# Kernel tuning notes

Hardware: AMD Instinct MI355X
Metric: run time of the kernel (lower is better)

## Reference

```python
import jax, jax.numpy as jnp
import numpy as np

N_ROW = 50000
N_COL = 50000
E = 600000
D = 128
NEG_SLOPE = 0.01  # torch LeakyReLU default


def _leaky(x):
    return jnp.where(x >= 0, x, NEG_SLOPE * x)


def _mlp(x, W1, b1, W2, b2):
    # (Linear -> LeakyReLU) x2, matching nn.Sequential in Conv_layer
    h = _leaky(x @ W1 + b1)
    return _leaky(h @ W2 + b2)


def setup_inputs() -> dict:
    key = jax.random.key(0)
    ks = jax.random.split(key, 16)
    inp = {
        "feat_row": jax.random.normal(ks[0], (N_ROW, D), jnp.float32),
        "feat_col": jax.random.normal(ks[1], (N_COL, D), jnp.float32),
        "src_c2r": jax.random.randint(ks[2], (E,), 0, N_COL, jnp.int32),
        "dst_c2r": jax.random.randint(ks[3], (E,), 0, N_ROW, jnp.int32),
        "w_c2r": jax.random.uniform(ks[4], (E,), jnp.float32),
        "src_r2c": jax.random.randint(ks[5], (E,), 0, N_ROW, jnp.int32),
        "dst_r2c": jax.random.randint(ks[6], (E,), 0, N_COL, jnp.int32),
        "w_r2c": jax.random.uniform(ks[7], (E,), jnp.float32),
        "W1_c2r": jax.random.normal(ks[8], (D, D), jnp.float32) / np.sqrt(D),
        "b1_c2r": jax.random.normal(ks[9], (D,), jnp.float32) * 0.01,
        "W2_c2r": jax.random.normal(ks[10], (D, D), jnp.float32) / np.sqrt(D),
        "b2_c2r": jax.random.normal(ks[11], (D,), jnp.float32) * 0.01,
        "W1_r2c": jax.random.normal(ks[12], (D, D), jnp.float32) / np.sqrt(D),
        "b1_r2c": jax.random.normal(ks[13], (D,), jnp.float32) * 0.01,
        "W2_r2c": jax.random.normal(ks[14], (D, D), jnp.float32) / np.sqrt(D),
        "b2_r2c": jax.random.normal(ks[15], (D,), jnp.float32) * 0.01,
        "eps_c2r": jnp.zeros((), jnp.float32),  # DGL GINConv init_eps=0
        "eps_r2c": jnp.zeros((), jnp.float32),
    }
    return inp


def reference(feat_row, feat_col, src_c2r, dst_c2r, w_c2r, src_r2c, dst_r2c, w_r2c,
              W1_c2r, b1_c2r, W2_c2r, b2_c2r, W1_r2c, b1_r2c, W2_r2c, b2_r2c,
              eps_c2r, eps_r2c):
    # col -> row GINConv (edge-weighted sum aggregation)
    msg = feat_col[src_c2r] * w_c2r[:, None]                       # [E, D]
    agg_row = jax.ops.segment_sum(msg, dst_c2r, num_segments=N_ROW)
    h_row = _mlp((1.0 + eps_c2r) * feat_row + agg_row, W1_c2r, b1_c2r, W2_c2r, b2_c2r)
    # row -> col GINConv using updated row features
    msg2 = h_row[src_r2c] * w_r2c[:, None]                         # [E, D]
    agg_col = jax.ops.segment_sum(msg2, dst_r2c, num_segments=N_COL)
    h_col = _mlp((1.0 + eps_r2c) * feat_col + agg_col, W1_r2c, b1_r2c, W2_r2c, b2_r2c)
    # residual (use_residual=True): add pre-conv embeddings
    return h_row + feat_row, h_col + feat_col
```

## Files before the change

### kernel.cpp

```cpp
#include <hip/hip_runtime.h>
#include <hip/hip_bf16.h>

#define NROW 50000
#define NCOL 50000
#define DDIM 128
#define CAP  32

typedef __bf16 bf16_t;
typedef __bf16 bf16x2 __attribute__((ext_vector_type(2)));
typedef __bf16 bf16x8 __attribute__((ext_vector_type(8)));
typedef float  f32x4  __attribute__((ext_vector_type(4)));

__device__ __forceinline__ float lrelu(float v) { return v >= 0.f ? v : 0.01f * v; }

__device__ __forceinline__ float ldf(const void* p, size_t i, bool f) {
    return f ? ((const float*)p)[i] : (float)((const bf16_t*)p)[i];
}

__device__ __forceinline__ bool dtf(const int* flags, int fi) {
    return (fi == -1) ? true : (fi == -2) ? false : (flags[fi] != 0);
}

struct TensorTab { const void* p[18]; int n[18]; };

__global__ __launch_bounds__(256) void detect_dtypes(TensorTab T, int* flags)
{
    __shared__ int vb, vf;
    const int tid = threadIdx.x;
    const int t = blockIdx.x;
    if (tid == 0) { vb = 0; vf = 0; }
    __syncthreads();
    const int n = T.n[t];
    const bool isFloatArr = (t != 2 && t != 3 && t != 5 && t != 6) && n >= 2;
    if (isFloatArr) {
        int nw = n / 2;
        int wi = (int)(((long long)tid * nw) >> 8);
        unsigned w = ((const unsigned*)T.p[t])[wi];
        unsigned low = w & 0xffffu;
        if (low) {
            int e = (int)((low >> 7) & 0xffu);
            if (e >= 90 && e <= 141) atomicAdd(&vb, 1);
            else                     atomicAdd(&vf, 1);
        }
    }
    __syncthreads();
    if (tid == 0) flags[t] = (isFloatArr && vf > vb) ? 1 : 0;
}

struct WPtrs { const void* W[4]; int fi[4]; };

__global__ __launch_bounds__(256) void prep_all(
    WPtrs P, const int* __restrict__ flags, __bf16* __restrict__ wfp,
    const void* __restrict__ feat, __bf16* __restrict__ cbuf, int n8, int fiFeat,
    int* __restrict__ zc, int zn, int cblocks, int zblocks)
{
    const int b = blockIdx.x;
    const int tid = threadIdx.x;
    if (b < cblocks) {
        int i = b * 256 + tid;
        if (i >= n8) return;
        const bool f = dtf(flags, fiFeat);
        bf16x8 v;
        if (f) {
            f32x4 a = ((const f32x4*)feat)[i * 2];
            f32x4 c = ((const f32x4*)feat)[i * 2 + 1];
#pragma unroll
            for (int j = 0; j < 4; ++j) { v[j] = (__bf16)a[j]; v[j + 4] = (__bf16)c[j]; }
        } else {
            v = ((const bf16x8*)feat)[i];
        }
        ((bf16x8*)cbuf)[i] = v;
    } else if (b < cblocks + zblocks) {
        int i = (b - cblocks) * 256 + tid;
        if (i < zn) zc[i] = 0;
    } else {
        int slot = (b - cblocks - zblocks) * 256 + tid;
        if (slot >= 4 * 2048) return;
        int m = slot >> 11, sIdx = slot & 2047;
        bool f = flags[P.fi[m]] != 0;
        int l = sIdx & 63, combo = sIdx >> 6;
        int ct = combo >> 2, kk = combo & 3;
        int col  = ct * 16 + (l & 15);
        int krow = kk * 32 + (l >> 4) * 8;
        bf16x8 v;
#pragma unroll
        for (int j = 0; j < 8; ++j)
            v[j] = (__bf16)ldf(P.W[m], (size_t)(krow + j) * DDIM + col, f);
        ((bf16x8*)wfp)[slot] = v;
    }
}

__global__ __launch_bounds__(256) void fill_slots_packed(
    const int* __restrict__ dst, const int* __restrict__ srcArr,
    const void* __restrict__ wArr, int nE, int* __restrict__ counts,
    int2* __restrict__ slots2, int* __restrict__ ovCount,
    int* __restrict__ ovList, float* __restrict__ agg,
    const int* __restrict__ flags, int fiW)
{
    int e = blockIdx.x * 256 + threadIdx.x;
    if (e >= nE) return;
    const bool fW = dtf(flags, fiW);
    int d = dst[e];
    int pos = atomicAdd(&counts[d], 1);
    if (pos < CAP) {
        int2 pk;
        pk.x = srcArr[e];
        pk.y = __float_as_int(ldf(wArr, e, fW));
        slots2[(size_t)d * CAP + pos] = pk;
    } else {
        if (pos == CAP) {
            f32x4 z = {0.f, 0.f, 0.f, 0.f};
            f32x4* rp = (f32x4*)(agg + (size_t)d * DDIM);
#pragma unroll 4
            for (int c = 0; c < DDIM / 4; ++c) rp[c] = z;
        }
        int k = atomicAdd(ovCount, 1);
        ovList[k] = e;
    }
}

__global__ __launch_bounds__(256) void segsum_ov(
    const __bf16* __restrict__ gsrc, const int* __restrict__ counts,
    const int2* __restrict__ slots2, float* __restrict__ agg, int nRows,
    const int* __restrict__ srcArr, const int* __restrict__ dstArr,
    const void* __restrict__ wArr, const int* __restrict__ ovList,
    const int* __restrict__ ovCount, const int* __restrict__ flags, int fiW,
    int gblocks)
{
    const int tid  = threadIdx.x;
    const int lane = tid & 63;

    if ((int)blockIdx.x >= gblocks) {
        const bool fW = dtf(flags, fiW);
        const int nOv = *ovCount;
        const int wv_ = tid >> 6;
        const int nWaves = 64 * 4;
        for (int k = (blockIdx.x - gblocks) * 4 + wv_; k < nOv; k += nWaves) {
            int e = ovList[k];
            int s = srcArr[e], d = dstArr[e];
            float wf = ldf(wArr, e, fW);
            bf16x2 v = ((const bf16x2*)gsrc)[(size_t)s * 64 + lane];
            float* ap = agg + (size_t)d * DDIM + lane * 2;
            unsafeAtomicAdd(ap + 0, (float)v[0] * wf);
            unsafeAtomicAdd(ap + 1, (float)v[1] * wf);
        }
        return;
    }

    int row = blockIdx.x * 4 + (tid >> 6);
    if (row >= nRows) return;

    int cntRaw = counts[row];
    int cnt = cntRaw > CAP ? CAP : cntRaw;

    int sr = 0; float wv = 0.f;
    if (lane < cnt) {
        int2 pk = slots2[(size_t)row * CAP + lane];
        sr = pk.x;
        wv = __int_as_float(pk.y);
    }

    float2* ap = (float2*)(agg + (size_t)row * DDIM) + lane;
    float2 acc0 = {0.f, 0.f}, acc1 = {0.f, 0.f};

    const bf16x2* fb = (const bf16x2*)gsrc;
    int i = 0;
    for (; i + 4 <= cnt; i += 4) {
        int   a0 = __shfl(sr, i),     a1 = __shfl(sr, i + 1);
        int   a2 = __shfl(sr, i + 2), a3 = __shfl(sr, i + 3);
        float w0 = __shfl(wv, i),     w1 = __shfl(wv, i + 1);
        float w2 = __shfl(wv, i + 2), w3 = __shfl(wv, i + 3);
        bf16x2 v0 = fb[(size_t)a0 * 64 + lane];
        bf16x2 v1 = fb[(size_t)a1 * 64 + lane];
        bf16x2 v2 = fb[(size_t)a2 * 64 + lane];
        bf16x2 v3 = fb[(size_t)a3 * 64 + lane];
        acc0.x += (float)v0[0] * w0; acc0.y += (float)v0[1] * w0;
        acc1.x += (float)v1[0] * w1; acc1.y += (float)v1[1] * w1;
        acc0.x += (float)v2[0] * w2; acc0.y += (float)v2[1] * w2;
        acc1.x += (float)v3[0] * w3; acc1.y += (float)v3[1] * w3;
    }
    for (; i < cnt; ++i) {
        int   a0 = __shfl(sr, i);
        float w0 = __shfl(wv, i);
        bf16x2 v0 = fb[(size_t)a0 * 64 + lane];
        acc0.x += (float)v0[0] * w0; acc0.y += (float)v0[1] * w0;
    }
    acc0.x += acc1.x; acc0.y += acc1.y;
    if (cntRaw > CAP) {
        unsafeAtomicAdd(&ap->x, acc0.x);
        unsafeAtomicAdd(&ap->y, acc0.y);
    } else {
        *ap = acc0;
    }
}

template <bool RESIDUAL, bool HOUT>
__global__ __launch_bounds__(256) void mlp_reg(
    const void* __restrict__ feat, const float* __restrict__ agg,
    const void* __restrict__ b1, const void* __restrict__ b2,
    const void* __restrict__ epsp, float* __restrict__ out, int N,
    const int* __restrict__ flags, int fiFeat, int fiB1, int fiB2, int fiEps,
    const __bf16* __restrict__ pW1, const __bf16* __restrict__ pW2,
    __bf16* __restrict__ hout, int* __restrict__ zc, int zn)
{
    __shared__ alignas(16) __bf16 h1t[64 * 136];

    const int tid  = threadIdx.x;
    if (zc) {
        int gi = blockIdx.x * 256 + tid;
        if (gi < zn) zc[gi] = 0;
    }

    const bool fF  = flags[fiFeat] != 0;
    const bool fB1 = flags[fiB1] != 0;
    const bool fB2 = flags[fiB2] != 0;
    const bool fE  = flags[fiEps] != 0;

    const int lane = tid & 63;
    const int wave = tid >> 6;
    const int quad = lane >> 4;
    const int r    = lane & 15;
    const int rowBase = blockIdx.x * 64 + wave * 16;

    const bf16x8* pw1v = (const bf16x8*)pW1;
    bf16x8 w1f[32];
#pragma unroll
    for (int i = 0; i < 32; ++i) w1f[i] = pw1v[i * 64 + lane];

    float bias1[8];
#pragma unroll
    for (int ct = 0; ct < 8; ++ct) bias1[ct] = ldf(b1, ct * 16 + r, fB1);
    const float eps1 = 1.f + ldf(epsp, 0, fE);

    bf16x8 a[4];
    {
        int rowA = rowBase + r;
        if (rowA < N) {
            size_t fb = (size_t)rowA * DDIM + quad * 8;
            const f32x4* gp = (const f32x4*)(agg + fb);
            if (fF) {
                const f32x4* fp = (const f32x4*)((const float*)feat + fb);
#pragma unroll
                for (int kk = 0; kk < 4; ++kk) {
                    f32x4 f0 = fp[kk * 8], f1 = fp[kk * 8 + 1];
                    f32x4 g0 = gp[kk * 8], g1 = gp[kk * 8 + 1];
                    bf16x8 av;
#pragma unroll
                    for (int j = 0; j < 4; ++j) {
                        av[j]     = (__bf16)(f0[j] * eps1 + g0[j]);
                        av[j + 4] = (__bf16)(f1[j] * eps1 + g1[j]);
                    }
                    a[kk] = av;
                }
            } else {
                const bf16x8* fp = (const bf16x8*)((const bf16_t*)feat + fb);
#pragma unroll
                for (int kk = 0; kk < 4; ++kk) {
                    bf16x8 fv = fp[kk * 4];
                    f32x4 g0 = gp[kk * 8], g1 = gp[kk * 8 + 1];
                    bf16x8 av;
#pragma unroll
                    for (int j = 0; j < 4; ++j) {
                        av[j]     = (__bf16)((float)fv[j]     * eps1 + g0[j]);
                        av[j + 4] = (__bf16)((float)fv[j + 4] * eps1 + g1[j]);
                    }
                    a[kk] = av;
                }
            }
        } else {
#pragma unroll
            for (int kk = 0; kk < 4; ++kk)
#pragma unroll
                for (int j = 0; j < 8; ++j) a[kk][j] = (__bf16)0.f;
        }
    }

#pragma unroll
    for (int ct = 0; ct < 8; ++ct) {
        f32x4 acc = {0.f, 0.f, 0.f, 0.f};
#pragma unroll
        for (int kk = 0; kk < 4; ++kk)
            acc = __builtin_amdgcn_mfma_f32_16x16x32_bf16(
                a[kk], w1f[ct * 4 + kk], acc, 0, 0, 0);
#pragma unroll
        for (int gg = 0; gg < 4; ++gg)
            h1t[(wave * 16 + quad * 4 + gg) * 136 + ct * 16 + r] =
                (__bf16)lrelu(acc[gg] + bias1[ct]);
    }

    bf16x8 a2[4];
#pragma unroll
    for (int kk = 0; kk < 4; ++kk)
        a2[kk] = *(const bf16x8*)&h1t[(wave * 16 + r) * 136 + kk * 32 + quad * 8];

    const bf16x8* pw2v = (const bf16x8*)pW2;
    bf16x8 w2f[32];
#pragma unroll
    for (int i = 0; i < 32; ++i) w2f[i] = pw2v[i * 64 + lane];
    float bias2[8];
#pragma unroll
    for (int ct = 0; ct < 8; ++ct) bias2[ct] = ldf(b2, ct * 16 + r, fB2);

#pragma unroll
    for (int ct = 0; ct < 8; ++ct) {
        f32x4 acc = {0.f, 0.f, 0.f, 0.f};
#pragma unroll
        for (int kk = 0; kk < 4; ++kk)
            acc = __builtin_amdgcn_mfma_f32_16x16x32_bf16(
                a2[kk], w2f[ct * 4 + kk], acc, 0, 0, 0);
#pragma unroll
        for (int gg = 0; gg < 4; ++gg) {
            int row = rowBase + quad * 4 + gg;
            float v = lrelu(acc[gg] + bias2[ct]);
            if (HOUT)
                h1t[(wave * 16 + quad * 4 + gg) * 136 + ct * 16 + r] = (__bf16)v;
            if (row < N) {
                int col = ct * 16 + r;
                if (RESIDUAL) v += ldf(feat, (size_t)row * DDIM + col, fF);
                out[(size_t)row * DDIM + col] = v;
            }
        }
    }

    if (HOUT) {
        __syncthreads();
        const int blockBase = blockIdx.x * 64;
#pragma unroll
        for (int c = 0; c < 4; ++c) {
            int chunk = tid + c * 256;
            int row = chunk >> 4;
            int k   = (chunk & 15) * 8;
            if (blockBase + row < N) {
                bf16x8 v = *(const bf16x8*)&h1t[row * 136 + k];
                *(bf16x8*)&hout[(size_t)(blockBase + row) * DDIM + k] = v;
            }
        }
    }
}

__global__ __launch_bounds__(256) void fill_slots(
    const int* __restrict__ dst, int nE, int* __restrict__ counts,
    int* __restrict__ slots, int* __restrict__ ovCount, int* __restrict__ ovList,
    const void* __restrict__ feat, const int* __restrict__ srcArr,
    const void* __restrict__ wArr, float* __restrict__ agg,
    const int* __restrict__ flags, int fiFeat, int fiW)
{
    int e = blockIdx.x * 256 + threadIdx.x;
    if (e >= nE) return;
    int d = dst[e];
    int pos = atomicAdd(&counts[d], 1);
    if (pos < CAP) {
        slots[(size_t)d * CAP + pos] = e;
    } else if (ovList) {
        int k = atomicAdd(ovCount, 1);
        ovList[k] = e;
    } else {
        const bool fF = dtf(flags, fiFeat);
        const bool fW = dtf(flags, fiW);
        int s = srcArr[e];
        float wf = ldf(wArr, e, fW);
        for (int c = 0; c < DDIM; ++c)
            unsafeAtomicAdd(&agg[(size_t)d * DDIM + c],
                            ldf(feat, (size_t)s * DDIM + c, fF) * wf);
    }
}

__global__ __launch_bounds__(256) void scatter_overflow(
    const void* __restrict__ feat, const int* __restrict__ srcArr,
    const int* __restrict__ dstArr, const void* __restrict__ wArr,
    const int* __restrict__ ovList, const int* __restrict__ ovCount,
    float* __restrict__ agg, const int* __restrict__ flags, int fiFeat, int fiW)
{
    const bool fF = dtf(flags, fiFeat);
    const bool fW = dtf(flags, fiW);
    const int nOv = *ovCount;
    const int stride = gridDim.x * 256;
    for (int g = blockIdx.x * 256 + threadIdx.x; (g >> 5) < nOv; g += stride) {
        int idx = g >> 5;
        int e = ovList[idx];
        int c = (g & 31) << 2;
        int s = srcArr[e], d = dstArr[e];
        float wf = ldf(wArr, e, fW);
        size_t base = (size_t)s * DDIM + c;
        float* ap = agg + (size_t)d * DDIM + c;
        unsafeAtomicAdd(ap + 0, ldf(feat, base + 0, fF) * wf);
        unsafeAtomicAdd(ap + 1, ldf(feat, base + 1, fF) * wf);
        unsafeAtomicAdd(ap + 2, ldf(feat, base + 2, fF) * wf);
        unsafeAtomicAdd(ap + 3, ldf(feat, base + 3, fF) * wf);
    }
}

template <bool ZINIT>
__global__ __launch_bounds__(256) void segsum(
    const void* __restrict__ feat, const int* __restrict__ srcArr,
    const void* __restrict__ wArr, const int* __restrict__ counts,
    const int* __restrict__ slots, float* __restrict__ agg, int nRows,
    const int* __restrict__ flags, int fiFeat, int fiW)
{
    const bool fF = dtf(flags, fiFeat);
    const bool fW = dtf(flags, fiW);
    int row = blockIdx.x * 4 + (threadIdx.x >> 6);
    if (row >= nRows) return;
    int lane = threadIdx.x & 63;

    int cnt = counts[row]; if (cnt > CAP) cnt = CAP;

    int sr = 0; float wv = 0.f;
    if (lane < cnt) {
        int e = slots[(size_t)row * CAP + lane];
        sr = srcArr[e];
        wv = ldf(wArr, e, fW);
    }

    float2* ap = (float2*)(agg + (size_t)row * DDIM) + lane;
    float2 acc0 = {0.f, 0.f}, acc1 = {0.f, 0.f};
    if (!ZINIT) acc0 = *ap;

    if (fF) {
        const float2* fb = (const float2*)feat;
        int i = 0;
        for (; i + 4 <= cnt; i += 4) {
            int   a0 = __shfl(sr, i),     a1 = __shfl(sr, i + 1);
            int   a2 = __shfl(sr, i + 2), a3 = __shfl(sr, i + 3);
            float w0 = __shfl(wv, i),     w1 = __shfl(wv, i + 1);
            float w2 = __shfl(wv, i + 2), w3 = __shfl(wv, i + 3);
            float2 v0 = fb[(size_t)a0 * 64 + lane];
            float2 v1 = fb[(size_t)a1 * 64 + lane];
            float2 v2 = fb[(size_t)a2 * 64 + lane];
            float2 v3 = fb[(size_t)a3 * 64 + lane];
            acc0.x += v0.x * w0; acc0.y += v0.y * w0;
            acc1.x += v1.x * w1; acc1.y += v1.y * w1;
            acc0.x += v2.x * w2; acc0.y += v2.y * w2;
            acc1.x += v3.x * w3; acc1.y += v3.y * w3;
        }
        for (; i < cnt; ++i) {
            int   a0 = __shfl(sr, i);
            float w0 = __shfl(wv, i);
            float2 v0 = fb[(size_t)a0 * 64 + lane];
            acc0.x += v0.x * w0; acc0.y += v0.y * w0;
        }
    } else {
        const bf16x2* fb = (const bf16x2*)feat;
        int i = 0;
        for (; i + 4 <= cnt; i += 4) {
            int   a0 = __shfl(sr, i),     a1 = __shfl(sr, i + 1);
            int   a2 = __shfl(sr, i + 2), a3 = __shfl(sr, i + 3);
            float w0 = __shfl(wv, i),     w1 = __shfl(wv, i + 1);
            float w2 = __shfl(wv, i + 2), w3 = __shfl(wv, i + 3);
            bf16x2 v0 = fb[(size_t)a0 * 64 + lane];
            bf16x2 v1 = fb[(size_t)a1 * 64 + lane];
            bf16x2 v2 = fb[(size_t)a2 * 64 + lane];
            bf16x2 v3 = fb[(size_t)a3 * 64 + lane];
            acc0.x += (float)v0[0] * w0; acc0.y += (float)v0[1] * w0;
            acc1.x += (float)v1[0] * w1; acc1.y += (float)v1[1] * w1;
            acc0.x += (float)v2[0] * w2; acc0.y += (float)v2[1] * w2;
            acc1.x += (float)v3[0] * w3; acc1.y += (float)v3[1] * w3;
        }
        for (; i < cnt; ++i) {
            int   a0 = __shfl(sr, i);
            float w0 = __shfl(wv, i);
            bf16x2 v0 = fb[(size_t)a0 * 64 + lane];
            acc0.x += (float)v0[0] * w0; acc0.y += (float)v0[1] * w0;
        }
    }
    acc0.x += acc1.x; acc0.y += acc1.y;
    *ap = acc0;
}

__global__ __launch_bounds__(256) void scatter_any(
    const void* __restrict__ feat, const int* __restrict__ src,
    const int* __restrict__ dst, const void* __restrict__ w,
    float* __restrict__ agg, int nE,
    const int* __restrict__ flags, int fiFeat, int fiW)
{
    const bool fF = dtf(flags, fiFeat);
    const bool fW = dtf(flags, fiW);
    int g = blockIdx.x * 256 + threadIdx.x;
    int e = g >> 5;
    if (e >= nE) return;
    int c = (g & 31) << 2;
    int s = src[e], d = dst[e];
    float wf = ldf(w, e, fW);
    size_t base = (size_t)s * DDIM + c;
    float* ap = agg + (size_t)d * DDIM + c;
    unsafeAtomicAdd(ap + 0, ldf(feat, base + 0, fF) * wf);
    unsafeAtomicAdd(ap + 1, ldf(feat, base + 1, fF) * wf);
    unsafeAtomicAdd(ap + 2, ldf(feat, base + 2, fF) * wf);
    unsafeAtomicAdd(ap + 3, ldf(feat, base + 3, fF) * wf);
}

__global__ __launch_bounds__(256) void residual_add(
    float* __restrict__ out, const void* __restrict__ feat, int n4,
    const int* __restrict__ flags, int fiFeat)
{
    const bool fF = flags[fiFeat] != 0;
    int i = blockIdx.x * 256 + threadIdx.x;
    if (i >= n4) return;
    f32x4 o = ((const f32x4*)out)[i];
    f32x4 r;
#pragma unroll
    for (int j = 0; j < 4; ++j) r[j] = o[j] + ldf(feat, (size_t)i * 4 + j, fF);
    ((f32x4*)out)[i] = r;
}

__device__ __forceinline__ void fill_wfrag(const void* __restrict__ W, bool f,
                                           __bf16* wf, int tid)
{
#pragma unroll
    for (int i = 0; i < 8; ++i) {
        int sIdx  = tid + i * 256;
        int l     = sIdx & 63;
        int combo = sIdx >> 6;
        int ct = combo >> 2, kk = combo & 3;
        int col  = ct * 16 + (l & 15);
        int krow = kk * 32 + (l >> 4) * 8;
        __bf16* dp = wf + (size_t)sIdx * 8;
#pragma unroll
        for (int j = 0; j < 8; ++j)
            dp[j] = (__bf16)ldf(W, (size_t)(krow + j) * DDIM + col, f);
    }
}

__device__ __forceinline__ void copy_wfrag(const __bf16* __restrict__ prep,
                                           __bf16* wf, int tid)
{
    const f32x4* sp = (const f32x4*)prep;
    f32x4* dp = (f32x4*)wf;
#pragma unroll
    for (int i = 0; i < 8; ++i) dp[tid + i * 256] = sp[tid + i * 256];
}

template <bool RESIDUAL, bool PREP>
__global__ __launch_bounds__(256) void mlp_kernel(
    const void* __restrict__ feat, const float* __restrict__ agg,
    const void* __restrict__ W1, const void* __restrict__ b1,
    const void* __restrict__ W2, const void* __restrict__ b2,
    const void* __restrict__ epsp, float* __restrict__ out, int N,
    const int* __restrict__ flags,
    int fiFeat, int fiW1, int fiB1, int fiW2, int fiB2, int fiEps,
    const __bf16* __restrict__ pW1, const __bf16* __restrict__ pW2)
{
    __shared__ alignas(16) __bf16 wf[32 * 64 * 8];
    __shared__ alignas(16) __bf16 h1t[64 * 136];

    const bool fF  = flags[fiFeat] != 0;
    const bool fB1 = flags[fiB1] != 0;
    const bool fB2 = flags[fiB2] != 0;
    const bool fE  = flags[fiEps] != 0;

    const int tid  = threadIdx.x;
    const int lane = tid & 63;
    const int wave = tid >> 6;
    const int quad = lane >> 4;
    const int r    = lane & 15;

    if (PREP) copy_wfrag(pW1, wf, tid);
    else      fill_wfrag(W1, flags[fiW1] != 0, wf, tid);

    const float eps1 = 1.f + ldf(epsp, 0, fE);
    const int rowBase = blockIdx.x * 64 + wave * 16;

    bf16x8 a[4];
    {
        int rowA = rowBase + r;
        if (rowA < N) {
            size_t fb = (size_t)rowA * DDIM + quad * 8;
            const f32x4* gp = (const f32x4*)(agg + fb);
            if (fF) {
                const f32x4* fp = (const f32x4*)((const float*)feat + fb);
#pragma unroll
                for (int kk = 0; kk < 4; ++kk) {
                    f32x4 f0 = fp[kk * 8], f1 = fp[kk * 8 + 1];
                    f32x4 g0 = gp[kk * 8], g1 = gp[kk * 8 + 1];
                    bf16x8 av;
#pragma unroll
                    for (int j = 0; j < 4; ++j) {
                        av[j]     = (__bf16)(f0[j] * eps1 + g0[j]);
                        av[j + 4] = (__bf16)(f1[j] * eps1 + g1[j]);
                    }
                    a[kk] = av;
                }
            } else {
                const bf16x8* fp = (const bf16x8*)((const bf16_t*)feat + fb);
#pragma unroll
                for (int kk = 0; kk < 4; ++kk) {
                    bf16x8 fv = fp[kk * 4];
                    f32x4 g0 = gp[kk * 8], g1 = gp[kk * 8 + 1];
                    bf16x8 av;
#pragma unroll
                    for (int j = 0; j < 4; ++j) {
                        av[j]     = (__bf16)((float)fv[j]     * eps1 + g0[j]);
                        av[j + 4] = (__bf16)((float)fv[j + 4] * eps1 + g1[j]);
                    }
                    a[kk] = av;
                }
            }
        } else {
#pragma unroll
            for (int kk = 0; kk < 4; ++kk)
#pragma unroll
                for (int j = 0; j < 8; ++j) a[kk][j] = (__bf16)0.f;
        }
    }

    __syncthreads();

    const bf16x8* wv = (const bf16x8*)wf;
#pragma unroll
    for (int ct = 0; ct < 8; ++ct) {
        f32x4 acc = {0.f, 0.f, 0.f, 0.f};
#pragma unroll
        for (int kk = 0; kk < 4; ++kk)
            acc = __builtin_amdgcn_mfma_f32_16x16x32_bf16(
                a[kk], wv[(ct * 4 + kk) * 64 + lane], acc, 0, 0, 0);
        float bias = ldf(b1, ct * 16 + r, fB1);
#pragma unroll
        for (int gg = 0; gg < 4; ++gg)
            h1t[(wave * 16 + quad * 4 + gg) * 136 + ct * 16 + r] =
                (__bf16)lrelu(acc[gg] + bias);
    }
    __syncthreads();

    bf16x8 a2[4];
#pragma unroll
    for (int kk = 0; kk < 4; ++kk)
        a2[kk] = *(const bf16x8*)&h1t[(wave * 16 + r) * 136 + kk * 32 + quad * 8];

    if (PREP) copy_wfrag(pW2, wf, tid);
    else      fill_wfrag(W2, flags[fiW2] != 0, wf, tid);
    __syncthreads();

#pragma unroll
    for (int ct = 0; ct < 8; ++ct) {
        f32x4 acc = {0.f, 0.f, 0.f, 0.f};
#pragma unroll
        for (int kk = 0; kk < 4; ++kk)
            acc = __builtin_amdgcn_mfma_f32_16x16x32_bf16(
                a2[kk], wv[(ct * 4 + kk) * 64 + lane], acc, 0, 0, 0);
        float bias = ldf(b2, ct * 16 + r, fB2);
#pragma unroll
        for (int gg = 0; gg < 4; ++gg) {
            int row = rowBase + quad * 4 + gg;
            if (row < N) {
                int col = ct * 16 + r;
                float v = lrelu(acc[gg] + bias);
                if (RESIDUAL) v += ldf(feat, (size_t)row * DDIM + col, fF);
                out[(size_t)row * DDIM + col] = v;
            }
        }
    }
}

extern "C" void kernel_launch(void* const* d_in, const int* in_sizes, int n_in,
                              void* d_out, int out_size, void* d_ws, size_t ws_size,
                              hipStream_t stream)
{
    const int* src_c2r = (const int*)d_in[2];
    const int* dst_c2r = (const int*)d_in[3];
    const int* src_r2c = (const int*)d_in[5];
    const int* dst_r2c = (const int*)d_in[6];
    const int nE = in_sizes[2];

    char* wsb = (char*)d_ws;
    int*    flags  = (int*)wsb;
    __bf16* wfprep = (__bf16*)(wsb + 128);
    int*    counts = (int*)(wsb + 128 + 131072);
    int*    ovCnt  = counts + NROW;
    size_t  ofs    = 128 + 131072 + ((size_t)NROW + 8) * 4;
    ofs = (ofs + 15) & ~(size_t)15;
    int2*   slots2 = (int2*)(wsb + ofs);
    int*    slots  = (int*)(wsb + ofs);
    size_t  ofsOvA = ofs + (size_t)NROW * CAP * 8;
    size_t  ofsOvB = ofs + (size_t)NROW * CAP * 4;
    int*    ovListA = (int*)(wsb + ofsOvA);
    int*    ovListB = (int*)(wsb + ofsOvB);
    size_t  ofsCb  = (ofsOvA + (size_t)nE * 4 + 15) & ~(size_t)15;
    __bf16* cbuf   = (__bf16*)(wsb + ofsCb);

    const size_t NEED_A  = ofsCb + (size_t)NROW * DDIM * 2;
    const size_t NEED_B  = ofsOvB + (size_t)nE * 4;
    const size_t NEED_B0 = ofsOvB;
    const bool tierA  = ws_size >= NEED_A;
    const bool tierB  = ws_size >= NEED_B;
    const bool tierB0 = ws_size >= NEED_B0;

    TensorTab T;
    for (int i = 0; i < 18; ++i) { T.p[i] = d_in[i]; T.n[i] = in_sizes[i]; }

    float* out_row = (float*)d_out;
    float* out_col = out_row + (size_t)NROW * DDIM;
    const size_t aggBytes = (size_t)NROW * DDIM * sizeof(float);

    const int eblocks  = (nE + 255) / 256;
    const int sblocks  = (nE * 32 + 255) / 256;
    const int mblocksR = (NROW + 63) / 64;
    const int mblocksC = (NCOL + 63) / 64;
    const int gblocksR = (NROW + 3) / 4;
    const int gblocksC = (NCOL + 3) / 4;
    const int cblocks  = (NCOL * DDIM / 8 + 255) / 256;
    const int zblocks  = ((NROW + 8) + 255) / 256;
    const int zn       = NROW + 8;

    detect_dtypes<<<18, 256, 0, stream>>>(T, flags);

    if (tierA) {
        WPtrs P;
        P.W[0] = d_in[8];  P.fi[0] = 8;
        P.W[1] = d_in[10]; P.fi[1] = 10;
        P.W[2] = d_in[12]; P.fi[2] = 12;
        P.W[3] = d_in[14]; P.fi[3] = 14;

        prep_all<<<cblocks + zblocks + 32, 256, 0, stream>>>(
            P, flags, wfprep, d_in[1], cbuf, NCOL * DDIM / 8, 1,
            counts, zn, cblocks, zblocks);

        fill_slots_packed<<<eblocks, 256, 0, stream>>>(dst_c2r, src_c2r,
            d_in[4], nE, counts, slots2, ovCnt, ovListA, out_col, flags, 4);
        segsum_ov<<<gblocksR + 64, 256, 0, stream>>>(cbuf, counts, slots2,
            out_col, NROW, src_c2r, dst_c2r, d_in[4], ovListA, ovCnt,
            flags, 4, gblocksR);
        mlp_reg<true, true><<<mblocksR, 256, 0, stream>>>(
            d_in[0], out_col, d_in[9], d_in[11], d_in[16],
            out_row, NROW, flags, 0, 9, 11, 16,
            wfprep + 0 * 16384, wfprep + 1 * 16384, cbuf, counts, zn);

        fill_slots_packed<<<eblocks, 256, 0, stream>>>(dst_r2c, src_r2c,
            d_in[7], nE, counts, slots2, ovCnt, ovListA, out_col, flags, 7);
        segsum_ov<<<gblocksC + 64, 256, 0, stream>>>(cbuf, counts, slots2,
            out_col, NCOL, src_r2c, dst_r2c, d_in[7], ovListA, ovCnt,
            flags, 7, gblocksC);
        mlp_reg<true, false><<<mblocksC, 256, 0, stream>>>(
            d_in[1], out_col, d_in[13], d_in[15], d_in[17],
            out_col, NCOL, flags, 1, 13, 15, 17,
            wfprep + 2 * 16384, wfprep + 3 * 16384, nullptr, nullptr, 0);
    } else if (tierB0) {
        WPtrs P;
        P.W[0] = d_in[8];  P.fi[0] = 8;
        P.W[1] = d_in[10]; P.fi[1] = 10;
        P.W[2] = d_in[12]; P.fi[2] = 12;
        P.W[3] = d_in[14]; P.fi[3] = 14;
        prep_all<<<32, 256, 0, stream>>>(P, flags, wfprep,
            nullptr, nullptr, 0, -1, nullptr, 0, 0, 0);

        hipMemsetAsync(counts, 0, ((size_t)NROW + 8) * 4, stream);
        if (!tierB) hipMemsetAsync(out_col, 0, aggBytes, stream);
        fill_slots<<<eblocks, 256, 0, stream>>>(dst_c2r, nE, counts, slots,
            ovCnt, tierB ? ovListB : nullptr,
            d_in[1], src_c2r, d_in[4], out_col, flags, 1, 4);
        if (tierB) {
            segsum<true><<<gblocksR, 256, 0, stream>>>(d_in[1], src_c2r,
                d_in[4], counts, slots, out_col, NROW, flags, 1, 4);
            scatter_overflow<<<256, 256, 0, stream>>>(d_in[1], src_c2r,
                dst_c2r, d_in[4], ovListB, ovCnt, out_col, flags, 1, 4);
        } else {
            segsum<false><<<gblocksR, 256, 0, stream>>>(d_in[1], src_c2r,
                d_in[4], counts, slots, out_col, NROW, flags, 1, 4);
        }
        mlp_kernel<false, true><<<mblocksR, 256, 0, stream>>>(
            d_in[0], out_col, d_in[8], d_in[9], d_in[10], d_in[11], d_in[16],
            out_row, NROW, flags, 0, 8, 9, 10, 11, 16,
            wfprep + 0 * 16384, wfprep + 1 * 16384);

        hipMemsetAsync(counts, 0, ((size_t)NROW + 8) * 4, stream);
        if (!tierB) hipMemsetAsync(out_col, 0, aggBytes, stream);
        fill_slots<<<eblocks, 256, 0, stream>>>(dst_r2c, nE, counts, slots,
            ovCnt, tierB ? ovListB : nullptr,
            out_row, src_r2c, d_in[7], out_col, flags, -1, 7);
        if (tierB) {
            segsum<true><<<gblocksC, 256, 0, stream>>>(out_row, src_r2c,
                d_in[7], counts, slots, out_col, NCOL, flags, -1, 7);
            scatter_overflow<<<256, 256, 0, stream>>>(out_row, src_r2c,
                dst_r2c, d_in[7], ovListB, ovCnt, out_col, flags, -1, 7);
        } else {
            segsum<false><<<gblocksC, 256, 0, stream>>>(out_row, src_r2c,
                d_in[7], counts, slots, out_col, NCOL, flags, -1, 7);
        }
        residual_add<<<(NROW * DDIM / 4 + 255) / 256, 256, 0, stream>>>(
            out_row, d_in[0], NROW * DDIM / 4, flags, 0);
        mlp_kernel<true, true><<<mblocksC, 256, 0, stream>>>(
            d_in[1], out_col, d_in[12], d_in[13], d_in[14], d_in[15], d_in[17],
            out_col, NCOL, flags, 1, 12, 13, 14, 15, 17,
            wfprep + 2 * 16384, wfprep + 3 * 16384);
    } else {
        hipMemsetAsync(out_col, 0, aggBytes, stream);
        scatter_any<<<sblocks, 256, 0, stream>>>(d_in[1], src_c2r, dst_c2r,
            d_in[4], out_col, nE, flags, 1, 4);
        mlp_kernel<false, false><<<mblocksR, 256, 0, stream>>>(
            d_in[0], out_col, d_in[8], d_in[9], d_in[10], d_in[11], d_in[16],
            out_row, NROW, flags, 0, 8, 9, 10, 11, 16, nullptr, nullptr);

        hipMemsetAsync(out_col, 0, aggBytes, stream);
        scatter_any<<<sblocks, 256, 0, stream>>>(out_row, src_r2c, dst_r2c,
            d_in[7], out_col, nE, flags, -1, 7);
        residual_add<<<(NROW * DDIM / 4 + 255) / 256, 256, 0, stream>>>(
            out_row, d_in[0], NROW * DDIM / 4, flags, 0);
        mlp_kernel<true, false><<<mblocksC, 256, 0, stream>>>(
            d_in[1], out_col, d_in[12], d_in[13], d_in[14], d_in[15], d_in[17],
            out_col, NCOL, flags, 1, 12, 13, 14, 15, 17, nullptr, nullptr);
    }
}
```

Before: 340.0 us.

## Fuse edge bucketing into prep and MLP kernels with separate count buffers

Adds a new top tier that keeps two count arrays and overflow lists, one per direction, so both are zeroed once inside the dtype-detect launch. The first direction's edge slot fill is folded into the weight/feature prep launch, and the second direction's fill runs as extra blocks of the first MLP kernel. The segment sum now handles overflow edges itself by scanning the overflow list, which removes the separate overflow kernel and the memset launches. The goal is fewer kernel launches and serialized passes. The cost is that rows with more than CAP edges scan the whole overflow list, and the workspace must be larger.

```diff
diff --git a/kernel.cpp b/kernel.cpp
--- a/kernel.cpp
+++ b/kernel.cpp
@@ -23,10 +23,16 @@
 
 struct TensorTab { const void* p[18]; int n[18]; };
 
-__global__ __launch_bounds__(256) void detect_dtypes(TensorTab T, int* flags)
-{
+__global__ __launch_bounds__(256) void detect_zero(TensorTab T, int* flags,
+                                                   int* z, int zn)
+{
+    const int tid = threadIdx.x;
+    if (blockIdx.x >= 18) {
+        int i = (blockIdx.x - 18) * 256 + tid;
+        if (i < zn) z[i] = 0;
+        return;
+    }
     __shared__ int vb, vf;
-    const int tid = threadIdx.x;
     const int t = blockIdx.x;
     if (tid == 0) { vb = 0; vf = 0; }
     __syncthreads();
@@ -47,7 +53,291 @@
     if (tid == 0) flags[t] = (isFloatArr && vf > vb) ? 1 : 0;
 }
 
+__device__ __forceinline__ void fill_edges(
+    int e, const int* __restrict__ dst, const int* __restrict__ srcArr,
+    const void* __restrict__ wArr, int nE, int* __restrict__ counts,
+    int2* __restrict__ slots2, int* __restrict__ ovCnt,
+    int* __restrict__ ovList, bool fW)
+{
+    if (e >= nE) return;
+    int d = dst[e];
+    int pos = atomicAdd(&counts[d], 1);
+    if (pos < CAP) {
+        int2 pk;
+        pk.x = srcArr[e];
+        pk.y = __float_as_int(ldf(wArr, e, fW));
+        slots2[(size_t)d * CAP + pos] = pk;
+    } else {
+        int k = atomicAdd(ovCnt, 1);
+        ovList[k] = e;
+    }
+}
+
 struct WPtrs { const void* W[4]; int fi[4]; };
+
+__global__ __launch_bounds__(256) void prep_fill(
+    WPtrs P, const int* __restrict__ flags, __bf16* __restrict__ wfp,
+    const void* __restrict__ feat, __bf16* __restrict__ cbuf, int n8,
+    int fiFeat, int cblocks,
+    const int* __restrict__ f_dst, const int* __restrict__ f_src,
+    const void* __restrict__ f_w, int f_nE, int* __restrict__ f_counts,
+    int2* __restrict__ f_slots2, int* __restrict__ f_ovCnt,
+    int* __restrict__ f_ovList, int f_fiW)
+{
+    const int b = blockIdx.x;
+    const int tid = threadIdx.x;
+    if (b < cblocks) {
+        int i = b * 256 + tid;
+        if (i >= n8) return;
+        const bool f = dtf(flags, fiFeat);
+        bf16x8 v;
+        if (f) {
+            f32x4 a = ((const f32x4*)feat)[i * 2];
+            f32x4 c = ((const f32x4*)feat)[i * 2 + 1];
+#pragma unroll
+            for (int j = 0; j < 4; ++j) { v[j] = (__bf16)a[j]; v[j + 4] = (__bf16)c[j]; }
+        } else {
+            v = ((const bf16x8*)feat)[i];
+        }
+        ((bf16x8*)cbuf)[i] = v;
+    } else if (b < cblocks + 32) {
+        int slot = (b - cblocks) * 256 + tid;
+        if (slot >= 4 * 2048) return;
+        int m = slot >> 11, sIdx = slot & 2047;
+        bool f = flags[P.fi[m]] != 0;
+        int l = sIdx & 63, combo = sIdx >> 6;
+        int ct = combo >> 2, kk = combo & 3;
+        int col  = ct * 16 + (l & 15);
+        int krow = kk * 32 + (l >> 4) * 8;
+        bf16x8 v;
+#pragma unroll
+        for (int j = 0; j < 8; ++j)
+            v[j] = (__bf16)ldf(P.W[m], (size_t)(krow + j) * DDIM + col, f);
+        ((bf16x8*)wfp)[slot] = v;
+    } else {
+        int e = (b - cblocks - 32) * 256 + tid;
+        fill_edges(e, f_dst, f_src, f_w, f_nE, f_counts, f_slots2,
+                   f_ovCnt, f_ovList, dtf(flags, f_fiW));
+    }
+}
+
+__global__ __launch_bounds__(256) void segsum_scan(
+    const __bf16* __restrict__ gsrc, const int* __restrict__ counts,
+    const int2* __restrict__ slots2, float* __restrict__ agg, int nRows,
+    const int* __restrict__ srcArr, const int* __restrict__ dstArr,
+    const void* __restrict__ wArr, const int* __restrict__ ovList,
+    const int* __restrict__ ovCount, const int* __restrict__ flags, int fiW)
+{
+    int row = blockIdx.x * 4 + (threadIdx.x >> 6);
+    if (row >= nRows) return;
+    int lane = threadIdx.x & 63;
+
+    int cntRaw = counts[row];
+    int cnt = cntRaw > CAP ? CAP : cntRaw;
+
+    int sr = 0; float wv = 0.f;
+    if (lane < cnt) {
+        int2 pk = slots2[(size_t)row * CAP + lane];
+        sr = pk.x;
+        wv = __int_as_float(pk.y);
+    }
+
+    float2* ap = (float2*)(agg + (size_t)row * DDIM) + lane;
+    float2 acc0 = {0.f, 0.f}, acc1 = {0.f, 0.f};
+
+    const bf16x2* fb = (const bf16x2*)gsrc;
+    int i = 0;
+    for (; i + 4 <= cnt; i += 4) {
+        int   a0 = __shfl(sr, i),     a1 = __shfl(sr, i + 1);
+        int   a2 = __shfl(sr, i + 2), a3 = __shfl(sr, i + 3);
+        float w0 = __shfl(wv, i),     w1 = __shfl(wv, i + 1);
+        float w2 = __shfl(wv, i + 2), w3 = __shfl(wv, i + 3);
+        bf16x2 v0 = fb[(size_t)a0 * 64 + lane];
+        bf16x2 v1 = fb[(size_t)a1 * 64 + lane];
+        bf16x2 v2 = fb[(size_t)a2 * 64 + lane];
+        bf16x2 v3 = fb[(size_t)a3 * 64 + lane];
+        acc0.x += (float)v0[0] * w0; acc0.y += (float)v0[1] * w0;
+        acc1.x += (float)v1[0] * w1; acc1.y += (float)v1[1] * w1;
+        acc0.x += (float)v2[0] * w2; acc0.y += (float)v2[1] * w2;
+        acc1.x += (float)v3[0] * w3; acc1.y += (float)v3[1] * w3;
+    }
+    for (; i < cnt; ++i) {
+        int   a0 = __shfl(sr, i);
+        float w0 = __shfl(wv, i);
+        bf16x2 v0 = fb[(size_t)a0 * 64 + lane];
+        acc0.x += (float)v0[0] * w0; acc0.y += (float)v0[1] * w0;
+    }
+    if (cntRaw > CAP) {
+        const bool fW = dtf(flags, fiW);
+        int nOv = *ovCount;
+        for (int k = 0; k < nOv; ++k) {
+            int e = ovList[k];
+            if (dstArr[e] == row) {
+                int s = srcArr[e];
+                float wf = ldf(wArr, e, fW);
+                bf16x2 v = fb[(size_t)s * 64 + lane];
+                acc0.x += (float)v[0] * wf; acc0.y += (float)v[1] * wf;
+            }
+        }
+    }
+    acc0.x += acc1.x; acc0.y += acc1.y;
+    *ap = acc0;
+}
+
+template <bool RESIDUAL, bool HOUT>
+__global__ __launch_bounds__(256) void mlp_reg(
+    const void* __restrict__ feat, const float* __restrict__ agg,
+    const void* __restrict__ b1, const void* __restrict__ b2,
+    const void* __restrict__ epsp, float* __restrict__ out, int N,
+    const int* __restrict__ flags, int fiFeat, int fiB1, int fiB2, int fiEps,
+    const __bf16* __restrict__ pW1, const __bf16* __restrict__ pW2,
+    __bf16* __restrict__ hout, int* __restrict__ zc, int zn,
+    int mblocks,
+    const int* __restrict__ f_dst, const int* __restrict__ f_src,
+    const void* __restrict__ f_w, int f_nE, int* __restrict__ f_counts,
+    int2* __restrict__ f_slots2, int* __restrict__ f_ovCnt,
+    int* __restrict__ f_ovList, int f_fiW)
+{
+    __shared__ alignas(16) __bf16 h1t[64 * 136];
+
+    const int tid  = threadIdx.x;
+    if (f_dst && (int)blockIdx.x >= mblocks) {
+        int e = ((int)blockIdx.x - mblocks) * 256 + tid;
+        fill_edges(e, f_dst, f_src, f_w, f_nE, f_counts, f_slots2,
+                   f_ovCnt, f_ovList, dtf(flags, f_fiW));
+        return;
+    }
+    if (zc) {
+        int gi = blockIdx.x * 256 + tid;
+        if (gi < zn) zc[gi] = 0;
+    }
+
+    const bool fF  = flags[fiFeat] != 0;
+    const bool fB1 = flags[fiB1] != 0;
+    const bool fB2 = flags[fiB2] != 0;
+    const bool fE  = flags[fiEps] != 0;
+
+    const int lane = tid & 63;
+    const int wave = tid >> 6;
+    const int quad = lane >> 4;
+    const int r    = lane & 15;
+    const int rowBase = blockIdx.x * 64 + wave * 16;
+
+    const bf16x8* pw1v = (const bf16x8*)pW1;
+    bf16x8 w1f[32];
+#pragma unroll
+    for (int i = 0; i < 32; ++i) w1f[i] = pw1v[i * 64 + lane];
+
+    float bias1[8];
+#pragma unroll
+    for (int ct = 0; ct < 8; ++ct) bias1[ct] = ldf(b1, ct * 16 + r, fB1);
+    const float eps1 = 1.f + ldf(epsp, 0, fE);
+
+    bf16x8 a[4];
+    {
+        int rowA = rowBase + r;
+        if (rowA < N) {
+            size_t fb = (size_t)rowA * DDIM + quad * 8;
+            const f32x4* gp = (const f32x4*)(agg + fb);
+            if (fF) {
+                const f32x4* fp = (const f32x4*)((const float*)feat + fb);
+#pragma unroll
+                for (int kk = 0; kk < 4; ++kk) {
+                    f32x4 f0 = fp[kk * 8], f1 = fp[kk * 8 + 1];
+                    f32x4 g0 = gp[kk * 8], g1 = gp[kk * 8 + 1];
+                    bf16x8 av;
+#pragma unroll
+                    for (int j = 0; j < 4; ++j) {
+                        av[j]     = (__bf16)(f0[j] * eps1 + g0[j]);
+                        av[j + 4] = (__bf16)(f1[j] * eps1 + g1[j]);
+                    }
+                    a[kk] = av;
+                }
+            } else {
+                const bf16x8* fp = (const bf16x8*)((const bf16_t*)feat + fb);
+#pragma unroll
+                for (int kk = 0; kk < 4; ++kk) {
+                    bf16x8 fv = fp[kk * 4];
+                    f32x4 g0 = gp[kk * 8], g1 = gp[kk * 8 + 1];
+                    bf16x8 av;
+#pragma unroll
+                    for (int j = 0; j < 4; ++j) {
+                        av[j]     = (__bf16)((float)fv[j]     * eps1 + g0[j]);
+                        av[j + 4] = (__bf16)((float)fv[j + 4] * eps1 + g1[j]);
+                    }
+                    a[kk] = av;
+                }
+            }
+        } else {
+#pragma unroll
+            for (int kk = 0; kk < 4; ++kk)
+#pragma unroll
+                for (int j = 0; j < 8; ++j) a[kk][j] = (__bf16)0.f;
+        }
+    }
+
+#pragma unroll
+    for (int ct = 0; ct < 8; ++ct) {
+        f32x4 acc = {0.f, 0.f, 0.f, 0.f};
+#pragma unroll
+        for (int kk = 0; kk < 4; ++kk)
+            acc = __builtin_amdgcn_mfma_f32_16x16x32_bf16(
+                a[kk], w1f[ct * 4 + kk], acc, 0, 0, 0);
+#pragma unroll
+        for (int gg = 0; gg < 4; ++gg)
+            h1t[(wave * 16 + quad * 4 + gg) * 136 + ct * 16 + r] =
+                (__bf16)lrelu(acc[gg] + bias1[ct]);
+    }
+
+    bf16x8 a2[4];
+#pragma unroll
+    for (int kk = 0; kk < 4; ++kk)
+        a2[kk] = *(const bf16x8*)&h1t[(wave * 16 + r) * 136 + kk * 32 + quad * 8];
+
+    const bf16x8* pw2v = (const bf16x8*)pW2;
+    bf16x8 w2f[32];
+#pragma unroll
+    for (int i = 0; i < 32; ++i) w2f[i] = pw2v[i * 64 + lane];
+    float bias2[8];
+#pragma unroll
+    for (int ct = 0; ct < 8; ++ct) bias2[ct] = ldf(b2, ct * 16 + r, fB2);
+
+#pragma unroll
+    for (int ct = 0; ct < 8; ++ct) {
+        f32x4 acc = {0.f, 0.f, 0.f, 0.f};
+#pragma unroll
+        for (int kk = 0; kk < 4; ++kk)
+            acc = __builtin_amdgcn_mfma_f32_16x16x32_bf16(
+                a2[kk], w2f[ct * 4 + kk], acc, 0, 0, 0);
+#pragma unroll
+        for (int gg = 0; gg < 4; ++gg) {
+            int row = rowBase + quad * 4 + gg;
+            float v = lrelu(acc[gg] + bias2[ct]);
+            if (HOUT)
+                h1t[(wave * 16 + quad * 4 + gg) * 136 + ct * 16 + r] = (__bf16)v;
+            if (row < N) {
+                int col = ct * 16 + r;
+                if (RESIDUAL) v += ldf(feat, (size_t)row * DDIM + col, fF);
+                out[(size_t)row * DDIM + col] = v;
+            }
+        }
+    }
+
+    if (HOUT) {
+        __syncthreads();
+        const int blockBase = blockIdx.x * 64;
+#pragma unroll
+        for (int c = 0; c < 4; ++c) {
+            int chunk = tid + c * 256;
+            int row = chunk >> 4;
+            int k   = (chunk & 15) * 8;
+            if (blockBase + row < N) {
+                bf16x8 v = *(const bf16x8*)&h1t[row * 136 + k];
+                *(bf16x8*)&hout[(size_t)(blockBase + row) * DDIM + k] = v;
+            }
+        }
+    }
+}
 
 __global__ __launch_bounds__(256) void prep_all(
     WPtrs P, const int* __restrict__ flags, __bf16* __restrict__ wfp,
@@ -194,279 +484,6 @@
     }
 }
 
-template <bool RESIDUAL, bool HOUT>
-__global__ __launch_bounds__(256) void mlp_reg(
-    const void* __restrict__ feat, const float* __restrict__ agg,
-    const void* __restrict__ b1, const void* __restrict__ b2,
-    const void* __restrict__ epsp, float* __restrict__ out, int N,
-    const int* __restrict__ flags, int fiFeat, int fiB1, int fiB2, int fiEps,
-    const __bf16* __restrict__ pW1, const __bf16* __restrict__ pW2,
-    __bf16* __restrict__ hout, int* __restrict__ zc, int zn)
-{
-    __shared__ alignas(16) __bf16 h1t[64 * 136];
-
-    const int tid  = threadIdx.x;
-    if (zc) {
-        int gi = blockIdx.x * 256 + tid;
-        if (gi < zn) zc[gi] = 0;
-    }
-
-    const bool fF  = flags[fiFeat] != 0;
-    const bool fB1 = flags[fiB1] != 0;
-    const bool fB2 = flags[fiB2] != 0;
-    const bool fE  = flags[fiEps] != 0;
-
-    const int lane = tid & 63;
-    const int wave = tid >> 6;
-    const int quad = lane >> 4;
-    const int r    = lane & 15;
-    const int rowBase = blockIdx.x * 64 + wave * 16;
-
-    const bf16x8* pw1v = (const bf16x8*)pW1;
-    bf16x8 w1f[32];
-#pragma unroll
-    for (int i = 0; i < 32; ++i) w1f[i] = pw1v[i * 64 + lane];
-
-    float bias1[8];
-#pragma unroll
-    for (int ct = 0; ct < 8; ++ct) bias1[ct] = ldf(b1, ct * 16 + r, fB1);
-    const float eps1 = 1.f + ldf(epsp, 0, fE);
-
-    bf16x8 a[4];
-    {
-        int rowA = rowBase + r;
-        if (rowA < N) {
-            size_t fb = (size_t)rowA * DDIM + quad * 8;
-            const f32x4* gp = (const f32x4*)(agg + fb);
-            if (fF) {
-                const f32x4* fp = (const f32x4*)((const float*)feat + fb);
-#pragma unroll
-                for (int kk = 0; kk < 4; ++kk) {
-                    f32x4 f0 = fp[kk * 8], f1 = fp[kk * 8 + 1];
-                    f32x4 g0 = gp[kk * 8], g1 = gp[kk * 8 + 1];
-                    bf16x8 av;
-#pragma unroll
-                    for (int j = 0; j < 4; ++j) {
-                        av[j]     = (__bf16)(f0[j] * eps1 + g0[j]);
-                        av[j + 4] = (__bf16)(f1[j] * eps1 + g1[j]);
-                    }
-                    a[kk] = av;
-                }
-            } else {
-                const bf16x8* fp = (const bf16x8*)((const bf16_t*)feat + fb);
-#pragma unroll
-                for (int kk = 0; kk < 4; ++kk) {
-                    bf16x8 fv = fp[kk * 4];
-                    f32x4 g0 = gp[kk * 8], g1 = gp[kk * 8 + 1];
-                    bf16x8 av;
-#pragma unroll
-                    for (int j = 0; j < 4; ++j) {
-                        av[j]     = (__bf16)((float)fv[j]     * eps1 + g0[j]);
-                        av[j + 4] = (__bf16)((float)fv[j + 4] * eps1 + g1[j]);
-                    }
-                    a[kk] = av;
-                }
-            }
-        } else {
-#pragma unroll
-            for (int kk = 0; kk < 4; ++kk)
-#pragma unroll
-                for (int j = 0; j < 8; ++j) a[kk][j] = (__bf16)0.f;
-        }
-    }
-
-#pragma unroll
-    for (int ct = 0; ct < 8; ++ct) {
-        f32x4 acc = {0.f, 0.f, 0.f, 0.f};
-#pragma unroll
-        for (int kk = 0; kk < 4; ++kk)
-            acc = __builtin_amdgcn_mfma_f32_16x16x32_bf16(
-                a[kk], w1f[ct * 4 + kk], acc, 0, 0, 0);
-#pragma unroll
-        for (int gg = 0; gg < 4; ++gg)
-            h1t[(wave * 16 + quad * 4 + gg) * 136 + ct * 16 + r] =
-                (__bf16)lrelu(acc[gg] + bias1[ct]);
-    }
-
-    bf16x8 a2[4];
-#pragma unroll
-    for (int kk = 0; kk < 4; ++kk)
-        a2[kk] = *(const bf16x8*)&h1t[(wave * 16 + r) * 136 + kk * 32 + quad * 8];
-
-    const bf16x8* pw2v = (const bf16x8*)pW2;
-    bf16x8 w2f[32];
-#pragma unroll
-    for (int i = 0; i < 32; ++i) w2f[i] = pw2v[i * 64 + lane];
-    float bias2[8];
-#pragma unroll
-    for (int ct = 0; ct < 8; ++ct) bias2[ct] = ldf(b2, ct * 16 + r, fB2);
-
-#pragma unroll
-    for (int ct = 0; ct < 8; ++ct) {
-        f32x4 acc = {0.f, 0.f, 0.f, 0.f};
-#pragma unroll
-        for (int kk = 0; kk < 4; ++kk)
-            acc = __builtin_amdgcn_mfma_f32_16x16x32_bf16(
-                a2[kk], w2f[ct * 4 + kk], acc, 0, 0, 0);
-#pragma unroll
-        for (int gg = 0; gg < 4; ++gg) {
-            int row = rowBase + quad * 4 + gg;
-            float v = lrelu(acc[gg] + bias2[ct]);
-            if (HOUT)
-                h1t[(wave * 16 + quad * 4 + gg) * 136 + ct * 16 + r] = (__bf16)v;
-            if (row < N) {
-                int col = ct * 16 + r;
-                if (RESIDUAL) v += ldf(feat, (size_t)row * DDIM + col, fF);
-                out[(size_t)row * DDIM + col] = v;
-            }
-        }
-    }
-
-    if (HOUT) {
-        __syncthreads();
-        const int blockBase = blockIdx.x * 64;
-#pragma unroll
-        for (int c = 0; c < 4; ++c) {
-            int chunk = tid + c * 256;
-            int row = chunk >> 4;
-            int k   = (chunk & 15) * 8;
-            if (blockBase + row < N) {
-                bf16x8 v = *(const bf16x8*)&h1t[row * 136 + k];
-                *(bf16x8*)&hout[(size_t)(blockBase + row) * DDIM + k] = v;
-            }
-        }
-    }
-}
-
-__global__ __launch_bounds__(256) void fill_slots(
-    const int* __restrict__ dst, int nE, int* __restrict__ counts,
-    int* __restrict__ slots, int* __restrict__ ovCount, int* __restrict__ ovList,
-    const void* __restrict__ feat, const int* __restrict__ srcArr,
-    const void* __restrict__ wArr, float* __restrict__ agg,
-    const int* __restrict__ flags, int fiFeat, int fiW)
-{
-    int e = blockIdx.x * 256 + threadIdx.x;
-    if (e >= nE) return;
-    int d = dst[e];
-    int pos = atomicAdd(&counts[d], 1);
-    if (pos < CAP) {
-        slots[(size_t)d * CAP + pos] = e;
-    } else if (ovList) {
-        int k = atomicAdd(ovCount, 1);
-        ovList[k] = e;
-    } else {
-        const bool fF = dtf(flags, fiFeat);
-        const bool fW = dtf(flags, fiW);
-        int s = srcArr[e];
-        float wf = ldf(wArr, e, fW);
-        for (int c = 0; c < DDIM; ++c)
-            unsafeAtomicAdd(&agg[(size_t)d * DDIM + c],
-                            ldf(feat, (size_t)s * DDIM + c, fF) * wf);
-    }
-}
-
-__global__ __launch_bounds__(256) void scatter_overflow(
-    const void* __restrict__ feat, const int* __restrict__ srcArr,
-    const int* __restrict__ dstArr, const void* __restrict__ wArr,
-    const int* __restrict__ ovList, const int* __restrict__ ovCount,
-    float* __restrict__ agg, const int* __restrict__ flags, int fiFeat, int fiW)
-{
-    const bool fF = dtf(flags, fiFeat);
-    const bool fW = dtf(flags, fiW);
-    const int nOv = *ovCount;
-    const int stride = gridDim.x * 256;
-    for (int g = blockIdx.x * 256 + threadIdx.x; (g >> 5) < nOv; g += stride) {
-        int idx = g >> 5;
-        int e = ovList[idx];
-        int c = (g & 31) << 2;
-        int s = srcArr[e], d = dstArr[e];
-        float wf = ldf(wArr, e, fW);
-        size_t base = (size_t)s * DDIM + c;
-        float* ap = agg + (size_t)d * DDIM + c;
-        unsafeAtomicAdd(ap + 0, ldf(feat, base + 0, fF) * wf);
-        unsafeAtomicAdd(ap + 1, ldf(feat, base + 1, fF) * wf);
-        unsafeAtomicAdd(ap + 2, ldf(feat, base + 2, fF) * wf);
-        unsafeAtomicAdd(ap + 3, ldf(feat, base + 3, fF) * wf);
-    }
-}
-
-template <bool ZINIT>
-__global__ __launch_bounds__(256) void segsum(
-    const void* __restrict__ feat, const int* __restrict__ srcArr,
-    const void* __restrict__ wArr, const int* __restrict__ counts,
-    const int* __restrict__ slots, float* __restrict__ agg, int nRows,
-    const int* __restrict__ flags, int fiFeat, int fiW)
-{
-    const bool fF = dtf(flags, fiFeat);
-    const bool fW = dtf(flags, fiW);
-    int row = blockIdx.x * 4 + (threadIdx.x >> 6);
-    if (row >= nRows) return;
-    int lane = threadIdx.x & 63;
-
-    int cnt = counts[row]; if (cnt > CAP) cnt = CAP;
-
-    int sr = 0; float wv = 0.f;
-    if (lane < cnt) {
-        int e = slots[(size_t)row * CAP + lane];
-        sr = srcArr[e];
-        wv = ldf(wArr, e, fW);
-    }
-
-    float2* ap = (float2*)(agg + (size_t)row * DDIM) + lane;
-    float2 acc0 = {0.f, 0.f}, acc1 = {0.f, 0.f};
-    if (!ZINIT) acc0 = *ap;
-
-    if (fF) {
-        const float2* fb = (const float2*)feat;
-        int i = 0;
-        for (; i + 4 <= cnt; i += 4) {
-            int   a0 = __shfl(sr, i),     a1 = __shfl(sr, i + 1);
-            int   a2 = __shfl(sr, i + 2), a3 = __shfl(sr, i + 3);
-            float w0 = __shfl(wv, i),     w1 = __shfl(wv, i + 1);
-            float w2 = __shfl(wv, i + 2), w3 = __shfl(wv, i + 3);
-            float2 v0 = fb[(size_t)a0 * 64 + lane];
-            float2 v1 = fb[(size_t)a1 * 64 + lane];
-            float2 v2 = fb[(size_t)a2 * 64 + lane];
-            float2 v3 = fb[(size_t)a3 * 64 + lane];
-            acc0.x += v0.x * w0; acc0.y += v0.y * w0;
-            acc1.x += v1.x * w1; acc1.y += v1.y * w1;
-            acc0.x += v2.x * w2; acc0.y += v2.y * w2;
-            acc1.x += v3.x * w3; acc1.y += v3.y * w3;
-        }
-        for (; i < cnt; ++i) {
-            int   a0 = __shfl(sr, i);
-            float w0 = __shfl(wv, i);
-            float2 v0 = fb[(size_t)a0 * 64 + lane];
-            acc0.x += v0.x * w0; acc0.y += v0.y * w0;
-        }
-    } else {
-        const bf16x2* fb = (const bf16x2*)feat;
-        int i = 0;
-        for (; i + 4 <= cnt; i += 4) {
-            int   a0 = __shfl(sr, i),     a1 = __shfl(sr, i + 1);
-            int   a2 = __shfl(sr, i + 2), a3 = __shfl(sr, i + 3);
-            float w0 = __shfl(wv, i),     w1 = __shfl(wv, i + 1);
-            float w2 = __shfl(wv, i + 2), w3 = __shfl(wv, i + 3);
-            bf16x2 v0 = fb[(size_t)a0 * 64 + lane];
-            bf16x2 v1 = fb[(size_t)a1 * 64 + lane];
-            bf16x2 v2 = fb[(size_t)a2 * 64 + lane];
-            bf16x2 v3 = fb[(size_t)a3 * 64 + lane];
-            acc0.x += (float)v0[0] * w0; acc0.y += (float)v0[1] * w0;
-            acc1.x += (float)v1[0] * w1; acc1.y += (float)v1[1] * w1;
-            acc0.x += (float)v2[0] * w2; acc0.y += (float)v2[1] * w2;
-            acc1.x += (float)v3[0] * w3; acc1.y += (float)v3[1] * w3;
-        }
-        for (; i < cnt; ++i) {
-            int   a0 = __shfl(sr, i);
-            float w0 = __shfl(wv, i);
-            bf16x2 v0 = fb[(size_t)a0 * 64 + lane];
-            acc0.x += (float)v0[0] * w0; acc0.y += (float)v0[1] * w0;
-        }
-    }
-    acc0.x += acc1.x; acc0.y += acc1.y;
-    *ap = acc0;
-}
-
 __global__ __launch_bounds__(256) void scatter_any(
     const void* __restrict__ feat, const int* __restrict__ src,
     const int* __restrict__ dst, const void* __restrict__ w,
@@ -521,24 +538,14 @@
     }
 }
 
-__device__ __forceinline__ void copy_wfrag(const __bf16* __restrict__ prep,
-                                           __bf16* wf, int tid)
-{
-    const f32x4* sp = (const f32x4*)prep;
-    f32x4* dp = (f32x4*)wf;
-#pragma unroll
-    for (int i = 0; i < 8; ++i) dp[tid + i * 256] = sp[tid + i * 256];
-}
-
-template <bool RESIDUAL, bool PREP>
+template <bool RESIDUAL>
 __global__ __launch_bounds__(256) void mlp_kernel(
     const void* __restrict__ feat, const float* __restrict__ agg,
     const void* __restrict__ W1, const void* __restrict__ b1,
     const void* __restrict__ W2, const void* __restrict__ b2,
     const void* __restrict__ epsp, float* __restrict__ out, int N,
     const int* __restrict__ flags,
-    int fiFeat, int fiW1, int fiB1, int fiW2, int fiB2, int fiEps,
-    const __bf16* __restrict__ pW1, const __bf16* __restrict__ pW2)
+    int fiFeat, int fiW1, int fiB1, int fiW2, int fiB2, int fiEps)
 {
     __shared__ alignas(16) __bf16 wf[32 * 64 * 8];
     __shared__ alignas(16) __bf16 h1t[64 * 136];
@@ -554,8 +561,7 @@
     const int quad = lane >> 4;
     const int r    = lane & 15;
 
-    if (PREP) copy_wfrag(pW1, wf, tid);
-    else      fill_wfrag(W1, flags[fiW1] != 0, wf, tid);
+    fill_wfrag(W1, flags[fiW1] != 0, wf, tid);
 
     const float eps1 = 1.f + ldf(epsp, 0, fE);
     const int rowBase = blockIdx.x * 64 + wave * 16;
@@ -626,8 +632,7 @@
     for (int kk = 0; kk < 4; ++kk)
         a2[kk] = *(const bf16x8*)&h1t[(wave * 16 + r) * 136 + kk * 32 + quad * 8];
 
-    if (PREP) copy_wfrag(pW2, wf, tid);
-    else      fill_wfrag(W2, flags[fiW2] != 0, wf, tid);
+    fill_wfrag(W2, flags[fiW2] != 0, wf, tid);
     __syncthreads();
 
 #pragma unroll
@@ -664,25 +669,33 @@
     char* wsb = (char*)d_ws;
     int*    flags  = (int*)wsb;
     __bf16* wfprep = (__bf16*)(wsb + 128);
+    int*    countsA = (int*)(wsb + 128 + 131072);
+    int*    ovCntA  = countsA + NROW;
+    int*    countsB = countsA + NROW + 8;
+    int*    ovCntB  = countsA + 2 * NROW + 8;
+    size_t  ofsA2   = 128 + 131072 + ((size_t)2 * NROW + 16) * 4;
+    ofsA2 = (ofsA2 + 15) & ~(size_t)15;
+    int2*   slots2A2  = (int2*)(wsb + ofsA2);
+    size_t  ofsOvA2   = ofsA2 + (size_t)NROW * CAP * 8;
+    int*    ovListA2  = (int*)(wsb + ofsOvA2);
+    int*    ovListB2  = ovListA2 + nE;
+    size_t  ofsCbA2   = (ofsOvA2 + (size_t)nE * 8 + 15) & ~(size_t)15;
+    __bf16* cbufA2    = (__bf16*)(wsb + ofsCbA2);
+    const size_t NEED_A2 = ofsCbA2 + (size_t)NROW * DDIM * 2;
+
     int*    counts = (int*)(wsb + 128 + 131072);
     int*    ovCnt  = counts + NROW;
     size_t  ofs    = 128 + 131072 + ((size_t)NROW + 8) * 4;
     ofs = (ofs + 15) & ~(size_t)15;
     int2*   slots2 = (int2*)(wsb + ofs);
-    int*    slots  = (int*)(wsb + ofs);
     size_t  ofsOvA = ofs + (size_t)NROW * CAP * 8;
-    size_t  ofsOvB = ofs + (size_t)NROW * CAP * 4;
     int*    ovListA = (int*)(wsb + ofsOvA);
-    int*    ovListB = (int*)(wsb + ofsOvB);
     size_t  ofsCb  = (ofsOvA + (size_t)nE * 4 + 15) & ~(size_t)15;
     __bf16* cbuf   = (__bf16*)(wsb + ofsCb);
-
-    const size_t NEED_A  = ofsCb + (size_t)NROW * DDIM * 2;
-    const size_t NEED_B  = ofsOvB + (size_t)nE * 4;
-    const size_t NEED_B0 = ofsOvB;
+    const size_t NEED_A = ofsCb + (size_t)NROW * DDIM * 2;
+
+    const bool tierA2 = ws_size >= NEED_A2;
     const bool tierA  = ws_size >= NEED_A;
-    const bool tierB  = ws_size >= NEED_B;
-    const bool tierB0 = ws_size >= NEED_B0;
 
     TensorTab T;
     for (int i = 0; i < 18; ++i) { T.p[i] = d_in[i]; T.n[i] = in_sizes[i]; }
@@ -698,22 +711,46 @@
     const int gblocksR = (NROW + 3) / 4;
     const int gblocksC = (NCOL + 3) / 4;
     const int cblocks  = (NCOL * DDIM / 8 + 255) / 256;
-    const int zblocks  = ((NROW + 8) + 255) / 256;
-    const int zn       = NROW + 8;
-
-    detect_dtypes<<<18, 256, 0, stream>>>(T, flags);
-
-    if (tierA) {
-        WPtrs P;
-        P.W[0] = d_in[8];  P.fi[0] = 8;
-        P.W[1] = d_in[10]; P.fi[1] = 10;
-        P.W[2] = d_in[12]; P.fi[2] = 12;
-        P.W[3] = d_in[14]; P.fi[3] = 14;
-
+
+    WPtrs P;
+    P.W[0] = d_in[8];  P.fi[0] = 8;
+    P.W[1] = d_in[10]; P.fi[1] = 10;
+    P.W[2] = d_in[12]; P.fi[2] = 12;
+    P.W[3] = d_in[14]; P.fi[3] = 14;
+
+    if (tierA2) {
+        const int zn2 = 2 * NROW + 16;
+        const int zb2 = (zn2 + 255) / 256;
+        detect_zero<<<18 + zb2, 256, 0, stream>>>(T, flags, countsA, zn2);
+        prep_fill<<<cblocks + 32 + eblocks, 256, 0, stream>>>(
+            P, flags, wfprep, d_in[1], cbufA2, NCOL * DDIM / 8, 1, cblocks,
+            dst_c2r, src_c2r, d_in[4], nE, countsA, slots2A2, ovCntA,
+            ovListA2, 4);
+        segsum_scan<<<gblocksR, 256, 0, stream>>>(cbufA2, countsA, slots2A2,
+            out_col, NROW, src_c2r, dst_c2r, d_in[4], ovListA2, ovCntA,
+            flags, 4);
+        mlp_reg<true, true><<<mblocksR + eblocks, 256, 0, stream>>>(
+            d_in[0], out_col, d_in[9], d_in[11], d_in[16],
+            out_row, NROW, flags, 0, 9, 11, 16,
+            wfprep + 0 * 16384, wfprep + 1 * 16384, cbufA2, nullptr, 0,
+            mblocksR, dst_r2c, src_r2c, d_in[7], nE, countsB, slots2A2,
+            ovCntB, ovListB2, 7);
+        segsum_scan<<<gblocksC, 256, 0, stream>>>(cbufA2, countsB, slots2A2,
+            out_col, NCOL, src_r2c, dst_r2c, d_in[7], ovListB2, ovCntB,
+            flags, 7);
+        mlp_reg<true, false><<<mblocksC, 256, 0, stream>>>(
+            d_in[1], out_col, d_in[13], d_in[15], d_in[17],
+            out_col, NCOL, flags, 1, 13, 15, 17,
+            wfprep + 2 * 16384, wfprep + 3 * 16384, nullptr, nullptr, 0,
+            mblocksC, nullptr, nullptr, nullptr, 0, nullptr, nullptr,
+            nullptr, nullptr, 0);
+    } else if (tierA) {
+        const int zblocks = ((NROW + 8) + 255) / 256;
+        const int zn      = NROW + 8;
+        detect_zero<<<18, 256, 0, stream>>>(T, flags, nullptr, 0);
         prep_all<<<cblocks + zblocks + 32, 256, 0, stream>>>(
             P, flags, wfprep, d_in[1], cbuf, NCOL * DDIM / 8, 1,
             counts, zn, cblocks, zblocks);
-
         fill_slots_packed<<<eblocks, 256, 0, stream>>>(dst_c2r, src_c2r,
             d_in[4], nE, counts, slots2, ovCnt, ovListA, out_col, flags, 4);
         segsum_ov<<<gblocksR + 64, 256, 0, stream>>>(cbuf, counts, slots2,
@@ -722,8 +759,9 @@
         mlp_reg<true, true><<<mblocksR, 256, 0, stream>>>(
             d_in[0], out_col, d_in[9], d_in[11], d_in[16],
             out_row, NROW, flags, 0, 9, 11, 16,
-            wfprep + 0 * 16384, wfprep + 1 * 16384, cbuf, counts, zn);
-
+            wfprep + 0 * 16384, wfprep + 1 * 16384, cbuf, counts, zn,
+            mblocksR, nullptr, nullptr, nullptr, 0, nullptr, nullptr,
+            nullptr, nullptr, 0);
         fill_slots_packed<<<eblocks, 256, 0, stream>>>(dst_r2c, src_r2c,
             d_in[7], nE, counts, slots2, ovCnt, ovListA, out_col, flags, 7);
         segsum_ov<<<gblocksC + 64, 256, 0, stream>>>(cbuf, counts, slots2,
@@ -732,70 +770,25 @@
         mlp_reg<true, false><<<mblocksC, 256, 0, stream>>>(
             d_in[1], out_col, d_in[13], d_in[15], d_in[17],
             out_col, NCOL, flags, 1, 13, 15, 17,
-            wfprep + 2 * 16384, wfprep + 3 * 16384, nullptr, nullptr, 0);
-    } else if (tierB0) {
-        WPtrs P;
-        P.W[0] = d_in[8];  P.fi[0] = 8;
-        P.W[1] = d_in[10]; P.fi[1] = 10;
-        P.W[2] = d_in[12]; P.fi[2] = 12;
-        P.W[3] = d_in[14]; P.fi[3] = 14;
-        prep_all<<<32, 256, 0, stream>>>(P, flags, wfprep,
-            nullptr, nullptr, 0, -1, nullptr, 0, 0, 0);
-
-        hipMemsetAsync(counts, 0, ((size_t)NROW + 8) * 4, stream);
-        if (!tierB) hipMemsetAsync(out_col, 0, aggBytes, stream);
-        fill_slots<<<eblocks, 256, 0, stream>>>(dst_c2r, nE, counts, slots,
-            ovCnt, tierB ? ovListB : nullptr,
-            d_in[1], src_c2r, d_in[4], out_col, flags, 1, 4);
-        if (tierB) {
-            segsum<true><<<gblocksR, 256, 0, stream>>>(d_in[1], src_c2r,
-                d_in[4], counts, slots, out_col, NROW, flags, 1, 4);
-            scatter_overflow<<<256, 256, 0, stream>>>(d_in[1], src_c2r,
-                dst_c2r, d_in[4], ovListB, ovCnt, out_col, flags, 1, 4);
-        } else {
-            segsum<false><<<gblocksR, 256, 0, stream>>>(d_in[1], src_c2r,
-                d_in[4], counts, slots, out_col, NROW, flags, 1, 4);
-        }
-        mlp_kernel<false, true><<<mblocksR, 256, 0, stream>>>(
-            d_in[0], out_col, d_in[8], d_in[9], d_in[10], d_in[11], d_in[16],
-            out_row, NROW, flags, 0, 8, 9, 10, 11, 16,
-            wfprep + 0 * 16384, wfprep + 1 * 16384);
-
-        hipMemsetAsync(counts, 0, ((size_t)NROW + 8) * 4, stream);
-        if (!tierB) hipMemsetAsync(out_col, 0, aggBytes, stream);
-        fill_slots<<<eblocks, 256, 0, stream>>>(dst_r2c, nE, counts, slots,
-            ovCnt, tierB ? ovListB : nullptr,
-            out_row, src_r2c, d_in[7], out_col, flags, -1, 7);
-        if (tierB) {
-            segsum<true><<<gblocksC, 256, 0, stream>>>(out_row, src_r2c,
-                d_in[7], counts, slots, out_col, NCOL, flags, -1, 7);
-            scatter_overflow<<<256, 256, 0, stream>>>(out_row, src_r2c,
-                dst_r2c, d_in[7], ovListB, ovCnt, out_col, flags, -1, 7);
-        } else {
-            segsum<false><<<gblocksC, 256, 0, stream>>>(out_row, src_r2c,
-                d_in[7], counts, slots, out_col, NCOL, flags, -1, 7);
-        }
-        residual_add<<<(NROW * DDIM / 4 + 255) / 256, 256, 0, stream>>>(
-            out_row, d_in[0], NROW * DDIM / 4, flags, 0);
-        mlp_kernel<true, true><<<mblocksC, 256, 0, stream>>>(
-            d_in[1], out_col, d_in[12], d_in[13], d_in[14], d_in[15], d_in[17],
-            out_col, NCOL, flags, 1, 12, 13, 14, 15, 17,
-            wfprep + 2 * 16384, wfprep + 3 * 16384);
+            wfprep + 2 * 16384, wfprep + 3 * 16384, nullptr, nullptr, 0,
+            mblocksC, nullptr, nullptr, nullptr, 0, nullptr, nullptr,
+            nullptr, nullptr, 0);
     } else {
+        detect_zero<<<18, 256, 0, stream>>>(T, flags, nullptr, 0);
         hipMemsetAsync(out_col, 0, aggBytes, stream);
         scatter_any<<<sblocks, 256, 0, stream>>>(d_in[1], src_c2r, dst_c2r,
             d_in[4], out_col, nE, flags, 1, 4);
-        mlp_kernel<false, false><<<mblocksR, 256, 0, stream>>>(
+        mlp_kernel<false><<<mblocksR, 256, 0, stream>>>(
             d_in[0], out_col, d_in[8], d_in[9], d_in[10], d_in[11], d_in[16],
-            out_row, NROW, flags, 0, 8, 9, 10, 11, 16, nullptr, nullptr);
+            out_row, NROW, flags, 0, 8, 9, 10, 11, 16);
 
         hipMemsetAsync(out_col, 0, aggBytes, stream);
         scatter_any<<<sblocks, 256, 0, stream>>>(out_row, src_r2c, dst_r2c,
             d_in[7], out_col, nE, flags, -1, 7);
         residual_add<<<(NROW * DDIM / 4 + 255) / 256, 256, 0, stream>>>(
             out_row, d_in[0], NROW * DDIM / 4, flags, 0);
-        mlp_kernel<true, false><<<mblocksC, 256, 0, stream>>>(
+        mlp_kernel<true><<<mblocksC, 256, 0, stream>>>(
             d_in[1], out_col, d_in[12], d_in[13], d_in[14], d_in[15], d_in[17],
-            out_col, NCOL, flags, 1, 12, 13, 14, 15, 17, nullptr, nullptr);
-    }
-}
+            out_col, NCOL, flags, 1, 12, 13, 14, 15, 17);
+    }
+}
```

Result: faster. 326.2 us (-4.1%).
